# Kernel tuning notes

Hardware: AMD Instinct MI355X
Metric: run time of the kernel (lower is better)

Reference implementation:

```python
import jax, jax.numpy as jnp
import numpy as np

# blueprint: (root_input_idx, children) where child >= 0 -> input[child], child < 0 -> hidden[-child-1]
BLUEPRINT = [(0, [0, 1, 2, 3]), (4, [4, 5, 6, 7]), (8, [8, 9, 10, 11]), (12, [12, 13, 14, 15]), (0, [-1, -2, -3, -4])]
B, T, V, E, H, TAGS = 32768, 16, 32000, 32, 64, 64


def setup_inputs() -> dict:
    key = jax.random.key(0)
    ks = jax.random.split(key, 13)
    x = jax.random.randint(ks[0], (B, T), 0, V)  # token ids (never hit pad row V)
    s = jax.random.randint(ks[1], (B,), 1, 5)    # lengths in [1, 4]
    sc = 0.125  # ~1/sqrt(H), matches torch LSTM uniform init scale
    emb = (jax.random.normal(ks[2], (V + 1, E), dtype=jnp.float32) * 0.1).at[V].set(0.0)
    Wih = jax.random.uniform(ks[3], (4 * H, E), minval=-sc, maxval=sc, dtype=jnp.float32)
    Whh = jax.random.uniform(ks[4], (4 * H, H), minval=-sc, maxval=sc, dtype=jnp.float32)
    bih = jax.random.uniform(ks[5], (4 * H,), minval=-sc, maxval=sc, dtype=jnp.float32)
    bhh = jax.random.uniform(ks[6], (4 * H,), minval=-sc, maxval=sc, dtype=jnp.float32)
    h0 = jax.random.uniform(ks[7], (H,), minval=-1.0, maxval=1.0, dtype=jnp.float32)
    c0 = jax.random.uniform(ks[8], (H,), minval=-1.0, maxval=1.0, dtype=jnp.float32)
    Wc = jax.random.uniform(ks[9], (E, H + E), minval=-0.1, maxval=0.1, dtype=jnp.float32)
    bc = jnp.zeros((E,), dtype=jnp.float32)
    Wt = jax.random.uniform(ks[10], (TAGS, E), minval=-0.18, maxval=0.18, dtype=jnp.float32)
    bt = jnp.zeros((TAGS,), dtype=jnp.float32)
    return {"x": x, "s": s, "emb": emb, "Wih": Wih, "Whh": Whh, "bih": bih, "bhh": bhh,
            "h0": h0, "c0": c0, "Wc": Wc, "bc": bc, "Wt": Wt, "bt": bt}


def _lstm_seq(cseq, h0b, c0b, Wih, Whh, b):
    # cseq: [B, L, E] -> outputs [B, L, H]; torch gate order i, f, g, o
    def step(carry, xt):
        h, cc = carry
        g = xt @ Wih.T + h @ Whh.T + b
        i, f, gg, o = jnp.split(g, 4, axis=-1)
        cc = jax.nn.sigmoid(f) * cc + jax.nn.sigmoid(i) * jnp.tanh(gg)
        h = jax.nn.sigmoid(o) * jnp.tanh(cc)
        return (h, cc), h
    _, hs = jax.lax.scan(step, (h0b, c0b), jnp.swapaxes(cseq, 0, 1))
    return jnp.swapaxes(hs, 0, 1)


def reference(x, s, emb, Wih, Whh, bih, bhh, h0, c0, Wc, bc, Wt, bt):
    bsz = x.shape[0]
    inputs = emb[x]  # [B, T, E]
    h0b = jnp.broadcast_to(h0[None, :], (bsz, h0.shape[0]))
    c0b = jnp.broadcast_to(c0[None, :], (bsz, c0.shape[0]))
    b = bih + bhh
    hidden = []
    for root, children in BLUEPRINT:
        r = inputs[:, root]  # [B, E]
        ch = [inputs[:, c] if c >= 0 else hidden[-c - 1] for c in children]
        cseq = jnp.stack(ch, axis=1)  # [B, L, E]
        L = cseq.shape[1]
        o = _lstm_seq(cseq, h0b, c0b, Wih, Whh, b)  # [B, L, H]
        # pack/pad semantics: positions t >= s[b] are zero after pad_packed; relu(0)=0
        mask = (jnp.arange(L)[None, :] < s[:, None]).astype(o.dtype)
        o = jax.nn.relu(o) * mask[..., None]
        last = o[:, -1]  # [B, H] (zero where s[b] < L, matching torch)
        comb = jax.nn.relu(jnp.concatenate([r, last], axis=1) @ Wc.T + bc)  # [B, E]
        hidden.append(comb)
    logits = hidden[-1] @ Wt.T + bt  # [B, TAGS]
    return jax.nn.log_softmax(logits, axis=1)
```

## Files before the change

kernel.cpp:

```cpp
#include <hip/hip_runtime.h>

#define NB 32768
#define NT 16
#define NV 32001
#define NE 32
#define NTAGS 64

typedef __attribute__((ext_vector_type(8))) short short8;
typedef __attribute__((ext_vector_type(4))) float f4;

#define MFMA16(a, b, c) __builtin_amdgcn_mfma_f32_16x16x32_bf16(a, b, c, 0, 0, 0)
#define CFENCE() asm volatile("" ::: "memory")
#define LDSSYNC() asm volatile("s_waitcnt lgkmcnt(0)" ::: "memory")

__device__ __forceinline__ float sigm_(float x) {
    return __builtin_amdgcn_rcpf(1.0f + __expf(-x));
}
__device__ __forceinline__ float tanh2_(float x) {
    float e = __expf(-2.0f * x);
    return fmaf(2.0f, __builtin_amdgcn_rcpf(1.0f + e), -1.0f);
}
__device__ __forceinline__ short f2bf(float x) {
    union { float f; unsigned u; } v; v.f = x;
    unsigned r = v.u + 0x7fffu + ((v.u >> 16) & 1u);
    return (short)(r >> 16);
}
__device__ __forceinline__ void pk2bf(float a, float b, short& lo, short& hi) {
    unsigned r;
    asm("v_cvt_pk_bf16_f32 %0, %1, %2" : "=v"(r) : "v"(a), "v"(b));
    lo = (short)r;
    hi = (short)(r >> 16);
}

__global__ __launch_bounds__(1024) void classify_prep(
    const int* __restrict__ s, const float* __restrict__ emb,
    const float* __restrict__ Wih, const float* __restrict__ Whh,
    const float* __restrict__ bih, const float* __restrict__ bhh,
    const float* __restrict__ Wc, const float* __restrict__ Wt,
    short* __restrict__ embH, short* __restrict__ wpack, short* __restrict__ wc1,
    short* __restrict__ wc2, short* __restrict__ wth, float* __restrict__ bsum,
    int* __restrict__ cH, int* __restrict__ listH, int* __restrict__ listL) {
    __shared__ int wbH[16], wbL[16];
    const int tid = threadIdx.x, b = blockIdx.x;
    if (b < 32) {
        const int row = b * 1024 + tid;
        const bool heavy = s[row] >= 4;
        unsigned long long mk = __ballot(heavy);
        const int wv = tid >> 6, ln = tid & 63;
        if (ln == 0) wbH[wv] = __popcll(mk);
        __syncthreads();
        if (tid == 0) {
            int tH = 0, tL = 0;
#pragma unroll
            for (int i = 0; i < 16; ++i) {
                int ch = wbH[i];
                wbH[i] = tH; wbL[i] = tL;
                tH += ch; tL += 64 - ch;
            }
            cH[b] = tH;
        }
        __syncthreads();
        unsigned long long ltm = (1ull << ln) - 1ull;
        if (heavy) listH[b * 1024 + wbH[wv] + __popcll(mk & ltm)] = row;
        else       listL[b * 1024 + wbL[wv] + __popcll((~mk) & ltm)] = row;
    }
    for (int i = b * 1024 + tid; i < NV * NE; i += 262144) embH[i] = f2bf(emb[i]);
    if (b == 32) {
        for (int t = tid; t < 18432; t += 1024) {
            int r = t / 72, c = t % 72;
            wpack[t] = f2bf(c < 64 ? Whh[r * 64 + c] : 0.f);
        }
        for (int t = tid; t < 10240; t += 1024) {
            int r = t / 40, c = t % 40;
            wpack[18432 + t] = f2bf(c < 32 ? Wih[r * 32 + c] : 0.f);
        }
        if (tid < 1024) { int r = tid >> 5, c = tid & 31; wc1[tid] = f2bf(Wc[r * 96 + c]); }
        for (int t = tid; t < 2048; t += 1024) {
            int r = t >> 6, c = t & 63;
            wc2[t] = f2bf(Wc[r * 96 + 32 + c]);
        }
        for (int t = tid; t < 2048; t += 1024) {
            int r = t >> 5, c = t & 31;
            wth[t] = f2bf(Wt[r * 32 + c]);
        }
        if (tid < 256) bsum[tid] = bih[tid] + bhh[tid];
    }
}

__global__ __launch_bounds__(256, 2) void main_fused(
    const int* __restrict__ x, const float* __restrict__ emb,
    const float* __restrict__ h0, const float* __restrict__ c0,
    const float* __restrict__ Wc, const float* __restrict__ bc,
    const float* __restrict__ Wt, const float* __restrict__ bt,
    const float* __restrict__ bsum,
    const short* __restrict__ wpack, const short* __restrict__ wc1,
    const short* __restrict__ wc2, const short* __restrict__ wth,
    const short* __restrict__ embH, const int* __restrict__ cH,
    const int* __restrict__ listH, const int* __restrict__ listL,
    float* __restrict__ out) {
    __shared__ __align__(16) short sWhh[18432];
    __shared__ __align__(16) short sWih[10240];
    __shared__ __align__(16) short sHA[4][16 * 72];
    __shared__ __align__(16) short sCmb[4][16 * 40];
    __shared__ __align__(16) short sC4[4][4 * 40];
    __shared__ int sRow[16];

    const int tid = threadIdx.x, wave = tid >> 6, lane = tid & 63;
    const int q = lane >> 4, n = lane & 15;
    const int NW = gridDim.x * 4;
    const int gw = blockIdx.x * 4 + wave;

    int cs = (lane < 32) ? cH[lane] : 0;
    int v = cs;
#pragma unroll
    for (int o = 1; o < 32; o <<= 1) { int t2 = __shfl_up(v, o); if (lane >= o) v += t2; }
    const int vIncl = v, vExcl = v - cs;
    const int nH = __shfl(vIncl, 31);
    const int nL = NB - nH;
    const int liIncl = (lane + 1) * 1024 - vIncl;
    const int liExcl = lane * 1024 - vExcl;
    const int nHB = (nH + 15) >> 4;
    const bool heavyBlk = (int)blockIdx.x < nHB;

    int row0 = 0, tokAll0 = 0;
    short8 aNext0;
    const int liBase = (n & 3) * 16 + (n >> 2) * 4;
    if (heavyBlk) {
        int idxq = min((int)blockIdx.x * 16 + wave * 4 + q, nH - 1);
        int sl = 0;
#pragma unroll
        for (int b2 = 0; b2 < 32; ++b2) sl += (__shfl(vIncl, b2) <= idxq) ? 1 : 0;
        row0 = listH[sl * 1024 + idxq - __shfl(vExcl, sl)];
        tokAll0 = x[row0 * 16 + n];
        aNext0 = *(const short8*)&embH[__shfl(tokAll0, liBase) * 32 + q * 8];
    }

    if (heavyBlk) {
        for (int i = tid; i < 2304; i += 256)
            ((uint4*)sWhh)[i] = ((const uint4*)wpack)[i];
        for (int i = tid; i < 1280; i += 256)
            ((uint4*)sWih)[i] = ((const uint4*)(wpack + 18432))[i];
        __syncthreads();
    }

    if (heavyBlk) {
        short* hA = sHA[wave];
        short* cmbB = sCmb[0];
        short* c4 = sC4[0];

        float bias16[16];
#pragma unroll
        for (int tl = 0; tl < 16; ++tl) bias16[tl] = bsum[tl * 16 + n];
        float bc2[2] = {bc[n], bc[16 + n]};
        float bt4[4] = {bt[n], bt[16 + n], bt[32 + n], bt[48 + n]};
        float c0v[4];
#pragma unroll
        for (int u = 0; u < 4; ++u) c0v[u] = c0[u * 16 + n];
        short8 h0f0, h0f1;
#pragma unroll
        for (int j = 0; j < 8; ++j) {
            h0f0[j] = f2bf(h0[q * 8 + j]);
            h0f1[j] = f2bf(h0[32 + q * 8 + j]);
        }
        const float c0w = c0[wave * 16 + n];

        const f4 zero4 = {0.f, 0.f, 0.f, 0.f};
        f4 acc[16];
        float cst[4][4];

        auto doStep = [&](short8 aP, short8 ah0, short8 ah1, bool doRelu) {
#pragma unroll
            for (int tl = 0; tl < 16; ++tl)
                acc[tl] = MFMA16(aP, *(const short8*)&sWih[(tl * 16 + n) * 40 + q * 8], zero4);
#pragma unroll
            for (int tl = 0; tl < 16; ++tl) {
                const short* rbp = &sWhh[(tl * 16 + n) * 72 + q * 8];
                f4 t0 = acc[tl];
                t0 = MFMA16(ah0, *(const short8*)rbp, t0);
                t0 = MFMA16(ah1, *(const short8*)(rbp + 32), t0);
                acc[tl] = t0;
            }
            CFENCE();
#pragma unroll
            for (int u = 0; u < 4; ++u) {
                float hv[4];
#pragma unroll
                for (int r = 0; r < 4; ++r) {
                    float ip = acc[u][r] + bias16[u];
                    float fp = acc[4 + u][r] + bias16[4 + u];
                    float gp = acc[8 + u][r] + bias16[8 + u];
                    float op = acc[12 + u][r] + bias16[12 + u];
                    float cc = fmaf(sigm_(fp), cst[r][u], sigm_(ip) * tanh2_(gp));
                    cst[r][u] = cc;
                    float hh = sigm_(op) * tanh2_(cc);
                    if (doRelu) hh = fmaxf(hh, 0.f);
                    hv[r] = hh;
                }
                short p0, p1, p2, p3;
                pk2bf(hv[0], hv[1], p0, p1);
                pk2bf(hv[2], hv[3], p2, p3);
                hA[(q * 4 + 0) * 72 + u * 16 + n] = p0;
                hA[(q * 4 + 1) * 72 + u * 16 + n] = p1;
                hA[(q * 4 + 2) * 72 + u * 16 + n] = p2;
                hA[(q * 4 + 3) * 72 + u * 16 + n] = p3;
            }
            CFENCE();
        };

#pragma unroll 1
        for (int itb = blockIdx.x; itb * 16 < nH; itb += (int)gridDim.x) {
            const int base = itb * 16;
            int row, tokAll;
            short8 aNext;
            if (itb == (int)blockIdx.x) {
                row = row0; tokAll = tokAll0; aNext = aNext0;
            } else {
                int idxq = min(base + wave * 4 + q, nH - 1);
                int sl = 0;
#pragma unroll
                for (int b2 = 0; b2 < 32; ++b2) sl += (__shfl(vIncl, b2) <= idxq) ? 1 : 0;
                row = listH[sl * 1024 + idxq - __shfl(vExcl, sl)];
                tokAll = x[row * 16 + n];
                aNext = *(const short8*)&embH[__shfl(tokAll, liBase) * 32 + q * 8];
            }
            if (n == 0) sRow[wave * 4 + q] = row;
            const int tokR0 = __shfl(tokAll, liBase);

#pragma unroll
            for (int u = 0; u < 4; ++u)
#pragma unroll
                for (int r = 0; r < 4; ++r) cst[r][u] = c0v[u];
            short8 a0 = h0f0, a1 = h0f1;
#pragma unroll 1
            for (int t = 0; t < 4; ++t) {
                short8 aP = aNext;
                if (t < 3) {
                    int tk2 = __shfl(tokAll, liBase + t + 1);
                    aNext = *(const short8*)&embH[tk2 * 32 + q * 8];
                }
                doStep(aP, a0, a1, t == 3);
                if (t < 3) {
                    a0 = *(const short8*)&hA[n * 72 + q * 8];
                    a1 = *(const short8*)&hA[n * 72 + 32 + q * 8];
                }
            }
            {
                short8 aRoot = *(const short8*)&embH[tokR0 * 32 + q * 8];
                short8 lh0 = *(const short8*)&hA[n * 72 + q * 8];
                short8 lh1 = *(const short8*)&hA[n * 72 + 32 + q * 8];
#pragma unroll
                for (int tl2 = 0; tl2 < 2; ++tl2) {
                    float bv = bc2[tl2];
                    f4 t0 = {bv, bv, bv, bv};
                    short8 b1 = *(const short8*)&wc1[(tl2 * 16 + n) * 32 + q * 8];
                    t0 = MFMA16(aRoot, b1, t0);
                    const short* rbp = &wc2[(tl2 * 16 + n) * 64 + q * 8];
                    t0 = MFMA16(lh0, *(const short8*)rbp, t0);
                    t0 = MFMA16(lh1, *(const short8*)(rbp + 32), t0);
                    short p0, p1, p2, p3;
                    pk2bf(fmaxf(t0[0], 0.f), fmaxf(t0[1], 0.f), p0, p1);
                    pk2bf(fmaxf(t0[2], 0.f), fmaxf(t0[3], 0.f), p2, p3);
                    short* db = &cmbB[(q * 16 + wave * 4) * 40 + tl2 * 16 + n];
                    db[0 * 40] = p0; db[1 * 40] = p1; db[2 * 40] = p2; db[3 * 40] = p3;
                }
            }
            float bias4[4];
            short8 wih2[4], whhA[4], whhB[4];
#pragma unroll
            for (int j = 0; j < 4; ++j) {
                bias4[j] = bsum[(j * 4 + wave) * 16 + n];
                wih2[j] = *(const short8*)&sWih[((j * 4 + wave) * 16 + n) * 40 + q * 8];
                const short* rbp = &sWhh[((j * 4 + wave) * 16 + n) * 72 + q * 8];
                whhA[j] = *(const short8*)rbp;
                whhB[j] = *(const short8*)(rbp + 32);
            }
            __syncthreads();

            {
                float cstw[4] = {c0w, c0w, c0w, c0w};
                short8 b0 = h0f0, b1 = h0f1;
                short8 aCp = *(const short8*)&cmbB[(0 * 16 + n) * 40 + q * 8];
#pragma unroll 1
                for (int t = 0; t < 4; ++t) {
                    short* hbw = (t & 1) ? sHA[1] : sHA[0];
                    short8 aC = aCp;
                    aCp = *(const short8*)&cmbB[(((t + 1) & 3) * 16 + n) * 40 + q * 8];
                    f4 ac4[4];
#pragma unroll
                    for (int j = 0; j < 4; ++j) ac4[j] = MFMA16(aC, wih2[j], zero4);
#pragma unroll
                    for (int j = 0; j < 4; ++j) {
                        f4 t0 = ac4[j];
                        t0 = MFMA16(b0, whhA[j], t0);
                        t0 = MFMA16(b1, whhB[j], t0);
                        ac4[j] = t0;
                    }
                    CFENCE();
                    float hv[4];
#pragma unroll
                    for (int r = 0; r < 4; ++r) {
                        float ip = ac4[0][r] + bias4[0];
                        float fp = ac4[1][r] + bias4[1];
                        float gp = ac4[2][r] + bias4[2];
                        float op = ac4[3][r] + bias4[3];
                        float cc = fmaf(sigm_(fp), cstw[r], sigm_(ip) * tanh2_(gp));
                        cstw[r] = cc;
                        float hh = sigm_(op) * tanh2_(cc);
                        if (t == 3) hh = fmaxf(hh, 0.f);
                        hv[r] = hh;
                    }
                    short p0, p1, p2, p3;
                    pk2bf(hv[0], hv[1], p0, p1);
                    pk2bf(hv[2], hv[3], p2, p3);
                    hbw[(q * 4 + 0) * 72 + wave * 16 + n] = p0;
                    hbw[(q * 4 + 1) * 72 + wave * 16 + n] = p1;
                    hbw[(q * 4 + 2) * 72 + wave * 16 + n] = p2;
                    hbw[(q * 4 + 3) * 72 + wave * 16 + n] = p3;
                    CFENCE();
                    __syncthreads();
                    b0 = *(const short8*)&hbw[n * 72 + q * 8];
                    b1 = *(const short8*)&hbw[n * 72 + 32 + q * 8];
                }
            }

            {
                const short* hL = sHA[1];
                int rv = sRow[n];
                int tokR = x[rv * 16];
                short8 aR = *(const short8*)&embH[tokR * 32 + q * 8];
                short8 lb0 = *(const short8*)&hL[n * 72 + q * 8];
                short8 lb1 = *(const short8*)&hL[n * 72 + 32 + q * 8];
#pragma unroll
                for (int tl2 = 0; tl2 < 2; ++tl2) {
                    float bv = bc2[tl2];
                    f4 t0 = {bv, bv, bv, bv};
                    short8 b1f = *(const short8*)&wc1[(tl2 * 16 + n) * 32 + q * 8];
                    t0 = MFMA16(aR, b1f, t0);
                    const short* rbp = &wc2[(tl2 * 16 + n) * 64 + q * 8];
                    t0 = MFMA16(lb0, *(const short8*)rbp, t0);
                    t0 = MFMA16(lb1, *(const short8*)(rbp + 32), t0);
                    if (q == wave) {
                        short p0, p1, p2, p3;
                        pk2bf(fmaxf(t0[0], 0.f), fmaxf(t0[1], 0.f), p0, p1);
                        pk2bf(fmaxf(t0[2], 0.f), fmaxf(t0[3], 0.f), p2, p3);
                        short* db = &c4[(wave * 4) * 40 + tl2 * 16 + n];
                        db[0 * 40] = p0; db[1 * 40] = p1; db[2 * 40] = p2; db[3 * 40] = p3;
                    }
                }
            }
            __syncthreads();

            {
                short8 cA = *(const short8*)&c4[n * 40 + q * 8];
                f4 a3[4];
#pragma unroll
                for (int tl3 = 0; tl3 < 4; ++tl3) {
                    float bv = bt4[tl3];
                    f4 t0 = {bv, bv, bv, bv};
                    short8 bW = *(const short8*)&wth[(tl3 * 16 + n) * 32 + q * 8];
                    a3[tl3] = MFMA16(cA, bW, t0);
                }
#pragma unroll
                for (int r = 0; r < 4; ++r) {
                    float l0 = a3[0][r], l1 = a3[1][r], l2 = a3[2][r], l3 = a3[3][r];
                    float mx = fmaxf(fmaxf(l0, l1), fmaxf(l2, l3));
#pragma unroll
                    for (int o2 = 8; o2; o2 >>= 1) mx = fmaxf(mx, __shfl_xor(mx, o2));
                    float sm = __expf(l0 - mx) + __expf(l1 - mx) +
                               __expf(l2 - mx) + __expf(l3 - mx);
#pragma unroll
                    for (int o2 = 8; o2; o2 >>= 1) sm += __shfl_xor(sm, o2);
                    float lse = mx + __logf(sm);
                    if (q == wave && base + wave * 4 + r < nH) {
                        int ro = sRow[wave * 4 + r];
                        out[ro * 64 + n] = l0 - lse;
                        out[ro * 64 + 16 + n] = l1 - lse;
                        out[ro * 64 + 32 + n] = l2 - lse;
                        out[ro * 64 + 48 + n] = l3 - lse;
                    }
                }
            }
        }
    }

    if (nL > 0) {
        const int lw = NW - 1 - gw;
        const int base0 = lw * 16;
        if (base0 < nL) {
            short* cmbL = sCmb[wave];
            f4 bcV[2], btV[4];
#pragma unroll
            for (int t = 0; t < 2; ++t) { float bv = bc[t * 16 + n]; bcV[t] = f4{bv, bv, bv, bv}; }
#pragma unroll
            for (int t = 0; t < 4; ++t) { float bv = bt[t * 16 + n]; btV[t] = f4{bv, bv, bv, bv}; }
#pragma unroll 1
            for (int base = base0; base < nL; base += NW * 16) {
                int idx = min(base + (lane & 15), nL - 1);
                int sl = 0;
#pragma unroll
                for (int b2 = 0; b2 < 32; ++b2) sl += (__shfl(liIncl, b2) <= idx) ? 1 : 0;
                const int lrow = listL[sl * 1024 + idx - __shfl(liExcl, sl)];
                const int ltok = x[lrow * 16];
                short8 aE = *(const short8*)&embH[__shfl(ltok, n) * 32 + q * 8];
#pragma unroll
                for (int tl2 = 0; tl2 < 2; ++tl2) {
                    short8 b1 = *(const short8*)&wc1[(tl2 * 16 + n) * 32 + q * 8];
                    f4 t0 = MFMA16(aE, b1, bcV[tl2]);
                    short p0, p1, p2, p3;
                    pk2bf(fmaxf(t0[0], 0.f), fmaxf(t0[1], 0.f), p0, p1);
                    pk2bf(fmaxf(t0[2], 0.f), fmaxf(t0[3], 0.f), p2, p3);
                    short* db = &cmbL[(q * 4) * 40 + tl2 * 16 + n];
                    db[0 * 40] = p0; db[1 * 40] = p1; db[2 * 40] = p2; db[3 * 40] = p3;
                }
                CFENCE();
                short8 cA = *(const short8*)&cmbL[n * 40 + q * 8];
                f4 a3[4];
#pragma unroll
                for (int tl3 = 0; tl3 < 4; ++tl3) {
                    short8 bW = *(const short8*)&wth[(tl3 * 16 + n) * 32 + q * 8];
                    a3[tl3] = MFMA16(cA, bW, btV[tl3]);
                }
#pragma unroll
                for (int r = 0; r < 4; ++r) {
                    float l0 = a3[0][r], l1 = a3[1][r], l2 = a3[2][r], l3 = a3[3][r];
                    float mx = fmaxf(fmaxf(l0, l1), fmaxf(l2, l3));
#pragma unroll
                    for (int o2 = 8; o2; o2 >>= 1) mx = fmaxf(mx, __shfl_xor(mx, o2));
                    float sm = __expf(l0 - mx) + __expf(l1 - mx) +
                               __expf(l2 - mx) + __expf(l3 - mx);
#pragma unroll
                    for (int o2 = 8; o2; o2 >>= 1) sm += __shfl_xor(sm, o2);
                    float lse = mx + __logf(sm);
                    int rowO = __shfl(lrow, q * 4 + r);
                    if (base + q * 4 + r < nL) {
                        out[rowO * 64 + n] = l0 - lse;
                        out[rowO * 64 + 16 + n] = l1 - lse;
                        out[rowO * 64 + 32 + n] = l2 - lse;
                        out[rowO * 64 + 48 + n] = l3 - lse;
                    }
                }
                CFENCE();
            }
        }
    }
}

__global__ __launch_bounds__(512) void tagger_fallback(
    const int* __restrict__ x, const int* __restrict__ s, const float* __restrict__ emb,
    const float* __restrict__ Wih, const float* __restrict__ Whh,
    const float* __restrict__ bih, const float* __restrict__ bhh,
    const float* __restrict__ h0, const float* __restrict__ c0,
    const float* __restrict__ Wc, const float* __restrict__ bc,
    const float* __restrict__ Wt, const float* __restrict__ bt,
    float* __restrict__ out) {
    __shared__ float4 WhhP[4096];
    __shared__ float combBuf[8][128];
    for (int i = threadIdx.x; i < 4096; i += 512) {
        int k = i & 63, jj = i >> 6;
        WhhP[k * 64 + jj] = make_float4(Whh[jj * 64 + k], Whh[(jj + 64) * 64 + k],
                                        Whh[(jj + 128) * 64 + k], Whh[(jj + 192) * 64 + k]);
    }
    __syncthreads();
    const int wave = threadIdx.x >> 6, j = threadIdx.x & 63, jm = j & 31;
    const int b = blockIdx.x * 8 + wave;
    const int sv = s[b];
    const int* xb = x + b * NT;
    const float bcj = bc[jm];
    auto rc_val = [&](int tok) -> float {
        float r = 0.f;
#pragma unroll
        for (int k = 0; k < 32; ++k) r = fmaf(emb[tok * NE + k], Wc[jm * 96 + k], r);
        return r;
    };
    float comb4;
    if (sv >= 4) {
        const float h0j = h0[j], c0j = c0[j];
        float4 bsj = make_float4(bih[j] + bhh[j], bih[j + 64] + bhh[j + 64],
                                 bih[j + 128] + bhh[j + 128], bih[j + 192] + bhh[j + 192]);
#pragma unroll 1
        for (int node = 0; node < 4; ++node) {
            float h = h0j, c = c0j;
#pragma unroll 1
            for (int t = 0; t < 4; ++t) {
                int tok = xb[node * 4 + t];
                float4 p = bsj;
#pragma unroll
                for (int k = 0; k < 32; ++k) {
                    float e = emb[tok * NE + k];
                    p.x = fmaf(e, Wih[j * 32 + k], p.x);
                    p.y = fmaf(e, Wih[(j + 64) * 32 + k], p.y);
                    p.z = fmaf(e, Wih[(j + 128) * 32 + k], p.z);
                    p.w = fmaf(e, Wih[(j + 192) * 32 + k], p.w);
                }
                float4 a = make_float4(0.f, 0.f, 0.f, 0.f);
#pragma unroll
                for (int k = 0; k < 64; ++k) {
                    float hk = __shfl(h, k);
                    float4 w = WhhP[k * 64 + j];
                    a.x = fmaf(hk, w.x, a.x); a.y = fmaf(hk, w.y, a.y);
                    a.z = fmaf(hk, w.z, a.z); a.w = fmaf(hk, w.w, a.w);
                }
                a.x += p.x; a.y += p.y; a.z += p.z; a.w += p.w;
                float ig = sigm_(a.x), fg = sigm_(a.y), gg = tanh2_(a.z), og = sigm_(a.w);
                c = fmaf(fg, c, ig * gg);
                h = og * tanh2_(c);
            }
            float last = fmaxf(h, 0.f);
            float acc = rc_val(xb[node * 4]) + bcj;
#pragma unroll
            for (int k = 0; k < 64; ++k)
                acc = fmaf(__shfl(last, k), Wc[jm * 96 + 32 + k], acc);
            if (j < 32) combBuf[wave][node * 32 + j] = fmaxf(acc, 0.f);
        }
        LDSSYNC();
        float h = h0j, c = c0j;
#pragma unroll 1
        for (int t = 0; t < 4; ++t) {
            float4 a = make_float4(0.f, 0.f, 0.f, 0.f);
#pragma unroll
            for (int k = 0; k < 32; ++k) {
                float ck = combBuf[wave][t * 32 + k];
                a.x = fmaf(ck, Wih[j * 32 + k], a.x);
                a.y = fmaf(ck, Wih[(j + 64) * 32 + k], a.y);
                a.z = fmaf(ck, Wih[(j + 128) * 32 + k], a.z);
                a.w = fmaf(ck, Wih[(j + 192) * 32 + k], a.w);
            }
#pragma unroll
            for (int k = 0; k < 64; ++k) {
                float hk = __shfl(h, k);
                float4 w = WhhP[k * 64 + j];
                a.x = fmaf(hk, w.x, a.x); a.y = fmaf(hk, w.y, a.y);
                a.z = fmaf(hk, w.z, a.z); a.w = fmaf(hk, w.w, a.w);
            }
            a.x += bih[j] + bhh[j]; a.y += bih[j + 64] + bhh[j + 64];
            a.z += bih[j + 128] + bhh[j + 128]; a.w += bih[j + 192] + bhh[j + 192];
            float ig = sigm_(a.x), fg = sigm_(a.y), gg = tanh2_(a.z), og = sigm_(a.w);
            c = fmaf(fg, c, ig * gg);
            h = og * tanh2_(c);
        }
        float last = fmaxf(h, 0.f);
        float acc = rc_val(xb[0]) + bcj;
#pragma unroll
        for (int k = 0; k < 64; ++k)
            acc = fmaf(__shfl(last, k), Wc[jm * 96 + 32 + k], acc);
        comb4 = fmaxf(acc, 0.f);
    } else {
        comb4 = fmaxf(rc_val(xb[0]) + bcj, 0.f);
    }
    float logit = bt[j];
    const float* wtr = Wt + j * 32;
#pragma unroll
    for (int k = 0; k < 32; ++k) logit = fmaf(__shfl(comb4, k), wtr[k], logit);
    float mx = logit;
#pragma unroll
    for (int off = 32; off; off >>= 1) mx = fmaxf(mx, __shfl_xor(mx, off));
    float ex = __expf(logit - mx);
    float sum = ex;
#pragma unroll
    for (int off = 32; off; off >>= 1) sum += __shfl_xor(sum, off);
    out[b * 64 + j] = logit - mx - __logf(sum);
}

extern "C" void kernel_launch(void* const* d_in, const int* in_sizes, int n_in,
                              void* d_out, int out_size, void* d_ws, size_t ws_size,
                              hipStream_t stream) {
    const int* x = (const int*)d_in[0];
    const int* s = (const int*)d_in[1];
    const float* emb = (const float*)d_in[2];
    const float* Wih = (const float*)d_in[3];
    const float* Whh = (const float*)d_in[4];
    const float* bih = (const float*)d_in[5];
    const float* bhh = (const float*)d_in[6];
    const float* h0 = (const float*)d_in[7];
    const float* c0 = (const float*)d_in[8];
    const float* Wc = (const float*)d_in[9];
    const float* bc = (const float*)d_in[10];
    const float* Wt = (const float*)d_in[11];
    const float* bt = (const float*)d_in[12];
    float* out = (float*)d_out;

    auto al16 = [](size_t v) { return (v + 15) & ~(size_t)15; };
    size_t off = 0;
    size_t oWpack = off; off = al16(off + (size_t)28672 * 2);
    size_t oWc1 = off;   off = al16(off + 1024 * 2);
    size_t oWc2 = off;   off = al16(off + 2048 * 2);
    size_t oWt = off;    off = al16(off + 2048 * 2);
    size_t oBsum = off;  off = al16(off + 256 * 4);
    size_t oEmbH = off;  off = al16(off + (size_t)NV * NE * 2);
    size_t oCH = off;    off = al16(off + 32 * 4);
    size_t oListH = off; off = al16(off + (size_t)NB * 4);
    size_t oListL = off; off = al16(off + (size_t)NB * 4);
    size_t need = off;

    char* ws = (char*)d_ws;
    if (ws_size >= need) {
        short* wpack = (short*)(ws + oWpack);
        short* wc1 = (short*)(ws + oWc1);
        short* wc2 = (short*)(ws + oWc2);
        short* wth = (short*)(ws + oWt);
        float* bsum = (float*)(ws + oBsum);
        short* embH = (short*)(ws + oEmbH);
        int* cHp = (int*)(ws + oCH);
        int* listH = (int*)(ws + oListH);
        int* listL = (int*)(ws + oListL);

        classify_prep<<<dim3(256), dim3(1024), 0, stream>>>(
            s, emb, Wih, Whh, bih, bhh, Wc, Wt,
            embH, wpack, wc1, wc2, wth, bsum, cHp, listH, listL);
        main_fused<<<dim3(512), dim3(256), 0, stream>>>(
            x, emb, h0, c0, Wc, bc, Wt, bt, bsum,
            wpack, wc1, wc2, wth, embH, cHp, listH, listL, out);
    } else {
        tagger_fallback<<<dim3(4096), dim3(512), 0, stream>>>(
            x, s, emb, Wih, Whh, bih, bhh, h0, c0, Wc, bc, Wt, bt, out);
    }
}
```

Baseline: 134.0 us.

## Drop LDS Wih copy, split LSTM step into halves, fold bias into exp2

```diff
diff --git a/kernel.cpp b/kernel.cpp
--- a/kernel.cpp
+++ b/kernel.cpp
@@ -13,6 +13,14 @@
 #define CFENCE() asm volatile("" ::: "memory")
 #define LDSSYNC() asm volatile("s_waitcnt lgkmcnt(0)" ::: "memory")
 
+#define NL2E  (-1.44269504f)
+#define NL2E2 (-2.88539008f)
+
+__device__ __forceinline__ float exp2_(float x) {
+    float r;
+    asm("v_exp_f32 %0, %1" : "=v"(r) : "v"(x));
+    return r;
+}
 __device__ __forceinline__ float sigm_(float x) {
     return __builtin_amdgcn_rcpf(1.0f + __expf(-x));
 }
@@ -99,7 +107,6 @@
     const int* __restrict__ listH, const int* __restrict__ listL,
     float* __restrict__ out) {
     __shared__ __align__(16) short sWhh[18432];
-    __shared__ __align__(16) short sWih[10240];
     __shared__ __align__(16) short sHA[4][16 * 72];
     __shared__ __align__(16) short sCmb[4][16 * 40];
     __shared__ __align__(16) short sC4[4][4 * 40];
@@ -121,6 +128,7 @@
     const int liExcl = lane * 1024 - vExcl;
     const int nHB = (nH + 15) >> 4;
     const bool heavyBlk = (int)blockIdx.x < nHB;
+    const short* wihG = wpack + 18432;
 
     int row0 = 0, tokAll0 = 0;
     short8 aNext0;
@@ -138,8 +146,6 @@
     if (heavyBlk) {
         for (int i = tid; i < 2304; i += 256)
             ((uint4*)sWhh)[i] = ((const uint4*)wpack)[i];
-        for (int i = tid; i < 1280; i += 256)
-            ((uint4*)sWih)[i] = ((const uint4*)(wpack + 18432))[i];
         __syncthreads();
     }
 
@@ -148,9 +154,10 @@
         short* cmbB = sCmb[0];
         short* c4 = sC4[0];
 
-        float bias16[16];
-#pragma unroll
-        for (int tl = 0; tl < 16; ++tl) bias16[tl] = bsum[tl * 16 + n];
+        float sb16[16];
+#pragma unroll
+        for (int tl = 0; tl < 16; ++tl)
+            sb16[tl] = (((tl >> 2) == 2) ? NL2E2 : NL2E) * bsum[tl * 16 + n];
         float bc2[2] = {bc[n], bc[16 + n]};
         float bt4[4] = {bt[n], bt[16 + n], bt[32 + n], bt[48 + n]};
         float c0v[4];
@@ -165,34 +172,47 @@
         const float c0w = c0[wave * 16 + n];
 
         const f4 zero4 = {0.f, 0.f, 0.f, 0.f};
-        f4 acc[16];
         float cst[4][4];
 
-        auto doStep = [&](short8 aP, short8 ah0, short8 ah1, bool doRelu) {
-#pragma unroll
-            for (int tl = 0; tl < 16; ++tl)
-                acc[tl] = MFMA16(aP, *(const short8*)&sWih[(tl * 16 + n) * 40 + q * 8], zero4);
-#pragma unroll
-            for (int tl = 0; tl < 16; ++tl) {
-                const short* rbp = &sWhh[(tl * 16 + n) * 72 + q * 8];
-                f4 t0 = acc[tl];
-                t0 = MFMA16(ah0, *(const short8*)rbp, t0);
-                t0 = MFMA16(ah1, *(const short8*)(rbp + 32), t0);
-                acc[tl] = t0;
-            }
+        auto halfStep = [&](int u0, short8 aP, short8 ah0, short8 ah1, bool doRelu) {
+            short8 wihF[8];
+#pragma unroll
+            for (int g = 0; g < 4; ++g)
+#pragma unroll
+                for (int k = 0; k < 2; ++k)
+                    wihF[g * 2 + k] =
+                        *(const short8*)&wihG[((g * 4 + u0 + k) * 16 + n) * 40 + q * 8];
+            f4 acc8[8];
+#pragma unroll
+            for (int j = 0; j < 8; ++j) acc8[j] = MFMA16(aP, wihF[j], zero4);
+#pragma unroll
+            for (int g = 0; g < 4; ++g)
+#pragma unroll
+                for (int k = 0; k < 2; ++k) {
+                    const short* rbp = &sWhh[((g * 4 + u0 + k) * 16 + n) * 72 + q * 8];
+                    f4 t0 = acc8[g * 2 + k];
+                    t0 = MFMA16(ah0, *(const short8*)rbp, t0);
+                    t0 = MFMA16(ah1, *(const short8*)(rbp + 32), t0);
+                    acc8[g * 2 + k] = t0;
+                }
             CFENCE();
 #pragma unroll
-            for (int u = 0; u < 4; ++u) {
+            for (int k = 0; k < 2; ++k) {
+                const int u = u0 + k;
                 float hv[4];
 #pragma unroll
                 for (int r = 0; r < 4; ++r) {
-                    float ip = acc[u][r] + bias16[u];
-                    float fp = acc[4 + u][r] + bias16[4 + u];
-                    float gp = acc[8 + u][r] + bias16[8 + u];
-                    float op = acc[12 + u][r] + bias16[12 + u];
-                    float cc = fmaf(sigm_(fp), cst[r][u], sigm_(ip) * tanh2_(gp));
+                    float si = __builtin_amdgcn_rcpf(
+                        1.0f + exp2_(fmaf(acc8[0 + k][r], NL2E, sb16[u])));
+                    float sf = __builtin_amdgcn_rcpf(
+                        1.0f + exp2_(fmaf(acc8[2 + k][r], NL2E, sb16[4 + u])));
+                    float tg = fmaf(2.0f, __builtin_amdgcn_rcpf(
+                        1.0f + exp2_(fmaf(acc8[4 + k][r], NL2E2, sb16[8 + u]))), -1.0f);
+                    float so = __builtin_amdgcn_rcpf(
+                        1.0f + exp2_(fmaf(acc8[6 + k][r], NL2E, sb16[12 + u])));
+                    float cc = fmaf(sf, cst[r][u], si * tg);
                     cst[r][u] = cc;
-                    float hh = sigm_(op) * tanh2_(cc);
+                    float hh = so * tanh2_(cc);
                     if (doRelu) hh = fmaxf(hh, 0.f);
                     hv[r] = hh;
                 }
@@ -238,7 +258,8 @@
                     int tk2 = __shfl(tokAll, liBase + t + 1);
                     aNext = *(const short8*)&embH[tk2 * 32 + q * 8];
                 }
-                doStep(aP, a0, a1, t == 3);
+                halfStep(0, aP, a0, a1, t == 3);
+                halfStep(2, aP, a0, a1, t == 3);
                 if (t < 3) {
                     a0 = *(const short8*)&hA[n * 72 + q * 8];
                     a1 = *(const short8*)&hA[n * 72 + 32 + q * 8];
@@ -264,12 +285,12 @@
                     db[0 * 40] = p0; db[1 * 40] = p1; db[2 * 40] = p2; db[3 * 40] = p3;
                 }
             }
-            float bias4[4];
+            float sb4[4];
             short8 wih2[4], whhA[4], whhB[4];
 #pragma unroll
             for (int j = 0; j < 4; ++j) {
-                bias4[j] = bsum[(j * 4 + wave) * 16 + n];
-                wih2[j] = *(const short8*)&sWih[((j * 4 + wave) * 16 + n) * 40 + q * 8];
+                sb4[j] = ((j == 2) ? NL2E2 : NL2E) * bsum[(j * 4 + wave) * 16 + n];
+                wih2[j] = *(const short8*)&wihG[((j * 4 + wave) * 16 + n) * 40 + q * 8];
                 const short* rbp = &sWhh[((j * 4 + wave) * 16 + n) * 72 + q * 8];
                 whhA[j] = *(const short8*)rbp;
                 whhB[j] = *(const short8*)(rbp + 32);
@@ -299,13 +320,17 @@
                     float hv[4];
 #pragma unroll
                     for (int r = 0; r < 4; ++r) {
-                        float ip = ac4[0][r] + bias4[0];
-                        float fp = ac4[1][r] + bias4[1];
-                        float gp = ac4[2][r] + bias4[2];
-                        float op = ac4[3][r] + bias4[3];
-                        float cc = fmaf(sigm_(fp), cstw[r], sigm_(ip) * tanh2_(gp));
+                        float si = __builtin_amdgcn_rcpf(
+                            1.0f + exp2_(fmaf(ac4[0][r], NL2E, sb4[0])));
+                        float sf = __builtin_amdgcn_rcpf(
+                            1.0f + exp2_(fmaf(ac4[1][r], NL2E, sb4[1])));
+                        float tg = fmaf(2.0f, __builtin_amdgcn_rcpf(
+                            1.0f + exp2_(fmaf(ac4[2][r], NL2E2, sb4[2]))), -1.0f);
+                        float so = __builtin_amdgcn_rcpf(
+                            1.0f + exp2_(fmaf(ac4[3][r], NL2E, sb4[3])));
+                        float cc = fmaf(sf, cstw[r], si * tg);
                         cstw[r] = cc;
-                        float hh = sigm_(op) * tanh2_(cc);
+                        float hh = so * tanh2_(cc);
                         if (t == 3) hh = fmaxf(hh, 0.f);
                         hv[r] = hh;
                     }
```

Result: no change. 131.6 us (-1.8%).
